# Performance work log

Hardware: AMD Instinct MI355X
Metric: run time of the kernel (lower is better)

Reference implementation:

```python
import jax, jax.numpy as jnp
import numpy as np
from jax import lax

CHUNK = 256  # points of the query set processed per step; intermediate is [B, CHUNK, M]


def _nn_min(x, y):
    """For each point in x [B,N,3], squared distance + index of nearest point in y [B,M,3].
    Chunked over N so the full [B,N,M] distance matrix is never materialized."""
    B, N, _ = x.shape
    y2 = jnp.sum(y * y, axis=-1)  # [B, M]
    K = N // CHUNK
    xr = jnp.swapaxes(x.reshape(B, K, CHUNK, 3), 0, 1)  # [K, B, CHUNK, 3]

    def chunk_fn(xc):  # xc: [B, CHUNK, 3]
        d = (jnp.sum(xc * xc, axis=-1)[..., None]
             - 2.0 * jnp.einsum('bcd,bmd->bcm', xc, y)
             + y2[:, None, :])  # [B, CHUNK, M]
        return jnp.min(d, axis=-1), jnp.argmin(d, axis=-1).astype(jnp.int32)

    dmin, idx = lax.map(chunk_fn, xr)  # [K, B, CHUNK]
    dmin = jnp.swapaxes(dmin, 0, 1).reshape(B, N)
    idx = jnp.swapaxes(idx, 0, 1).reshape(B, N)
    return dmin, idx


def setup_inputs() -> dict:
    key = jax.random.key(0)
    k1, k2 = jax.random.split(key)
    xyz1 = jax.random.normal(k1, (8, 16384, 3), dtype=jnp.float32)
    xyz2 = jax.random.normal(k2, (8, 16384, 3), dtype=jnp.float32)
    return {"xyz1": xyz1, "xyz2": xyz2}


def reference(xyz1, xyz2):
    dist1, idx1 = _nn_min(xyz1, xyz2)  # [B, N], [B, N]
    dist2, idx2 = _nn_min(xyz2, xyz1)  # [B, M], [B, M]
    return dist1, dist2, idx1, idx2
```

## Files before the change

### kernel.cpp

```cpp
#include <hip/hip_runtime.h>
#include <stdint.h>

#define BATCH 8
#define NPTS  16384
#define BN    (BATCH * NPTS)
#define NT    512
#define NTH   256
#define QPB   256
#define MARGIN 3.0e-3f

typedef float f32x16 __attribute__((ext_vector_type(16)));
typedef short s16x8  __attribute__((ext_vector_type(8)));

__device__ __forceinline__ uint16_t bfr(float x) {
    uint32_t u = __float_as_uint(x);
    return (uint16_t)((u + 0x7FFFu + ((u >> 16) & 1u)) >> 16);
}
__device__ __forceinline__ float bff(uint16_t s) {
    return __uint_as_float(((uint32_t)s) << 16);
}
__device__ __forceinline__ void split2(float v, uint16_t* a, uint16_t* b) {
    *a = bfr(v); *b = bfr(v - bff(*a));
}
__device__ __forceinline__ uint32_t pk2(uint16_t lo, uint16_t hi) {
    return (uint32_t)lo | ((uint32_t)hi << 16);
}
__device__ __forceinline__ uint32_t key32(float d) {
    uint32_t b = __float_as_uint(d);
    return (b & 0x80000000u) ? ~b : (b | 0x80000000u);
}
__device__ __forceinline__ float dec32(uint32_t k) {
    return __uint_as_float((k & 0x80000000u) ? (k ^ 0x80000000u) : ~k);
}

#define F16(M_) M_(0) M_(1) M_(2) M_(3) M_(4) M_(5) M_(6) M_(7) \
                M_(8) M_(9) M_(10) M_(11) M_(12) M_(13) M_(14) M_(15)

#define MIN3(a, b, c) fminf(fminf((a), (b)), (c))

__device__ __forceinline__ float fold16(const f32x16 a) {
    const float u0 = MIN3(a[0],  a[1],  a[2]);
    const float u1 = MIN3(a[3],  a[4],  a[5]);
    const float u2 = MIN3(a[6],  a[7],  a[8]);
    const float u3 = MIN3(a[9],  a[10], a[11]);
    const float u4 = MIN3(a[12], a[13], a[14]);
    const float v0 = MIN3(u0, u1, a[15]);
    const float v1 = MIN3(u2, u3, u4);
    return fminf(v0, v1);
}

__global__ __launch_bounds__(256) void enc_kernel(
    const float* __restrict__ Y, uint4* __restrict__ enc2,
    float4* __restrict__ y4)
{
#pragma clang fp contract(off)
    const int g = blockIdx.x * 256 + threadIdx.x;
    const int b = g >> 14, p = g & (NPTS - 1);
    const float y0 = Y[(size_t)g * 3 + 0];
    const float y1 = Y[(size_t)g * 3 + 1];
    const float y2 = Y[(size_t)g * 3 + 2];
    const float ys = (y0 * y0 + y1 * y1) + y2 * y2;
    uint16_t Ya, Yb; split2(ys, &Ya, &Yb);
    uint16_t H0, M0; split2(-2.0f * y0, &H0, &M0);
    uint16_t H1, M1; split2(-2.0f * y1, &H1, &M1);
    uint16_t H2, M2; split2(-2.0f * y2, &H2, &M2);
    const uint16_t ONE = 0x3F80;
    const int tile = p >> 5, col = p & 31;
    const size_t base = ((size_t)b * NT + tile) * 64;
    enc2[base + col]      = make_uint4(pk2(ONE, ONE), pk2(Ya, Yb), pk2(H0, M0), pk2(H0, M0));
    enc2[base + 32 + col] = make_uint4(pk2(H1, M1), pk2(H1, M1), pk2(H2, M2), pk2(H2, M2));
    y4[g] = make_float4(y0, y1, y2, ys);
}

#define MKQFR(dst, qq) { \
        const float* xp = Xp + (size_t)(qq) * 3; \
        const float x0 = xp[0], x1 = xp[1], x2 = xp[2]; \
        const float xs = (x0 * x0 + x1 * x1) + x2 * x2; \
        uint16_t Xa, Xb; split2(xs, &Xa, &Xb); \
        uint16_t h0, m0; split2(x0, &h0, &m0); \
        uint16_t h1, m1; split2(x1, &h1, &m1); \
        uint16_t h2, m2; split2(x2, &h2, &m2); \
        const uint16_t ONE = 0x3F80; \
        if (hi == 0) { \
            dst[0]=(short)Xa; dst[1]=(short)Xb; dst[2]=(short)ONE; dst[3]=(short)ONE; \
            dst[4]=(short)h0; dst[5]=(short)h0; dst[6]=(short)m0;  dst[7]=(short)m0; \
        } else { \
            dst[0]=(short)h1; dst[1]=(short)h1; dst[2]=(short)m1;  dst[3]=(short)m1; \
            dst[4]=(short)h2; dst[5]=(short)h2; dst[6]=(short)m2;  dst[7]=(short)m2; \
        } }

#define SWEEP_DECODE() \
    const int tid = threadIdx.x; \
    const int l   = tid & 63; \
    const int wv  = tid >> 6; \
    const int col = l & 31; \
    const int hi  = l >> 5; \
    const int batch = blockIdx.x & 7; \
    const int kh    = (blockIdx.x >> 3) & 1; \
    const int xblk  = blockIdx.x >> 4; \
    const int qbase = batch * NPTS + xblk * QPB + wv * 64; \
    const uint4* pb = enc2 + ((size_t)batch * NT + (size_t)kh * NTH) * 64;

__global__ __launch_bounds__(256, 4) void nn_sweep1(
    const float* __restrict__ Xp, const uint4* __restrict__ enc2,
    uint32_t* __restrict__ mkey)
{
#pragma clang fp contract(off)
    SWEEP_DECODE()

    const f32x16 zf = {0.f,0.f,0.f,0.f,0.f,0.f,0.f,0.f,
                       0.f,0.f,0.f,0.f,0.f,0.f,0.f,0.f};

    s16x8 qfr0, qfr1;
    MKQFR(qfr0, qbase + col)
    MKQFR(qfr1, qbase + 32 + col)

    float run0 = __builtin_inff(), run1 = __builtin_inff();

    uint4 n0 = pb[0 * 64 + l], n1 = pb[1 * 64 + l];
    uint4 n2 = pb[2 * 64 + l], n3 = pb[3 * 64 + l];
    for (int t = 0; t < NTH; t += 4) {
        const uint4 c0 = n0, c1 = n1, c2 = n2, c3 = n3;
        const uint4* nb = pb + (size_t)(t + 4) * 64;
        n0 = nb[0 * 64 + l]; n1 = nb[1 * 64 + l];
        n2 = nb[2 * 64 + l]; n3 = nb[3 * 64 + l];
#define S1T(cq) { \
        const s16x8 pA = __builtin_bit_cast(s16x8, cq); \
        const f32x16 a0 = __builtin_amdgcn_mfma_f32_32x32x16_bf16(pA, qfr0, zf, 0, 0, 0); \
        run0 = fminf(run0, fold16(a0)); \
        const f32x16 a1 = __builtin_amdgcn_mfma_f32_32x32x16_bf16(pA, qfr1, zf, 0, 0, 0); \
        run1 = fminf(run1, fold16(a1)); }
        S1T(c0) S1T(c1) S1T(c2) S1T(c3)
#undef S1T
    }
    run0 = fminf(run0, __shfl_xor(run0, 32, 64));
    run1 = fminf(run1, __shfl_xor(run1, 32, 64));
    if (hi == 0) {
        atomicMin(&mkey[qbase + col],      key32(run0));
        atomicMin(&mkey[qbase + 32 + col], key32(run1));
    }
}

__global__ __launch_bounds__(256, 4) void nn_sweep2(
    const float* __restrict__ Xp, const uint4* __restrict__ enc2,
    const float4* __restrict__ y4, const uint32_t* __restrict__ mkey,
    unsigned long long* __restrict__ gkeys)
{
#pragma clang fp contract(off)
    __shared__ unsigned long long keys[QPB];
    SWEEP_DECODE()

    const float4* Y4 = y4 + (size_t)batch * NPTS;

    keys[tid] = ~0ull;

    const f32x16 zf = {0.f,0.f,0.f,0.f,0.f,0.f,0.f,0.f,
                       0.f,0.f,0.f,0.f,0.f,0.f,0.f,0.f};

    int rowpack[4] = {0, 0, 0, 0};
    {
        s16x8 pa = {0,0,0,0,0,0,0,0}, pbq = {0,0,0,0,0,0,0,0};
        if (hi == 0) { pa[0] = (short)bfr((float)col); pbq[0] = (short)0x3F80; }
        const f32x16 rowp = __builtin_amdgcn_mfma_f32_32x32x16_bf16(pa, pbq, zf, 0, 0, 0);
#define PR(i) rowpack[(i) >> 2] |= ((int)rowp[i] & 0xFF) << (((i) & 3) * 8);
        F16(PR)
#undef PR
    }

    s16x8 qfr0, qfr1;
    float qa0, qa1, qa2, qas, qb0, qb1, qb2, qbs;
    {
        const float* xp = Xp + (size_t)(qbase + col) * 3;
        qa0 = xp[0]; qa1 = xp[1]; qa2 = xp[2];
        qas = (qa0 * qa0 + qa1 * qa1) + qa2 * qa2;
    }
    {
        const float* xp = Xp + (size_t)(qbase + 32 + col) * 3;
        qb0 = xp[0]; qb1 = xp[1]; qb2 = xp[2];
        qbs = (qb0 * qb0 + qb1 * qb1) + qb2 * qb2;
    }
    MKQFR(qfr0, qbase + col)
    MKQFR(qfr1, qbase + 32 + col)

    const float thr0 = dec32(mkey[qbase + col]) + MARGIN;
    const float thr1 = dec32(mkey[qbase + 32 + col]) + MARGIN;

    __syncthreads();

#define HITR(accv, jb, foff, thr, qx0, qx1, qx2, qxs, r) \
        if ((accv)[r] <= (thr)) { \
            const int jc = (jb) + ((rowpack[(r) >> 2] >> (((r) & 3) * 8)) & 0xFF); \
            const float4 yv = Y4[jc]; \
            const float dd = ((qxs) - 2.0f * (((qx0) * yv.x + (qx1) * yv.y) + (qx2) * yv.z)) + yv.w; \
            atomicMin(&keys[wv * 64 + (foff) + col], \
                      ((unsigned long long)key32(dd) << 32) | (uint32_t)jc); }
#define HIT(accv, jb, foff, thr, qx0, qx1, qx2, qxs) \
        if (fold16(accv) <= (thr)) { \
            HITR(accv, jb, foff, thr, qx0, qx1, qx2, qxs, 0) \
            HITR(accv, jb, foff, thr, qx0, qx1, qx2, qxs, 1) \
            HITR(accv, jb, foff, thr, qx0, qx1, qx2, qxs, 2) \
            HITR(accv, jb, foff, thr, qx0, qx1, qx2, qxs, 3) \
            HITR(accv, jb, foff, thr, qx0, qx1, qx2, qxs, 4) \
            HITR(accv, jb, foff, thr, qx0, qx1, qx2, qxs, 5) \
            HITR(accv, jb, foff, thr, qx0, qx1, qx2, qxs, 6) \
            HITR(accv, jb, foff, thr, qx0, qx1, qx2, qxs, 7) \
            HITR(accv, jb, foff, thr, qx0, qx1, qx2, qxs, 8) \
            HITR(accv, jb, foff, thr, qx0, qx1, qx2, qxs, 9) \
            HITR(accv, jb, foff, thr, qx0, qx1, qx2, qxs, 10) \
            HITR(accv, jb, foff, thr, qx0, qx1, qx2, qxs, 11) \
            HITR(accv, jb, foff, thr, qx0, qx1, qx2, qxs, 12) \
            HITR(accv, jb, foff, thr, qx0, qx1, qx2, qxs, 13) \
            HITR(accv, jb, foff, thr, qx0, qx1, qx2, qxs, 14) \
            HITR(accv, jb, foff, thr, qx0, qx1, qx2, qxs, 15) \
        }

    uint4 n0 = pb[0 * 64 + l], n1 = pb[1 * 64 + l];
    for (int t = 0; t < NTH; t += 2) {
        const uint4 c0 = n0, c1 = n1;
        const uint4* nb = pb + (size_t)(t + 2) * 64;
        n0 = nb[0 * 64 + l]; n1 = nb[1 * 64 + l];
#define S2T(cq, j) { \
        const s16x8 pA = __builtin_bit_cast(s16x8, cq); \
        const int jb = (kh * NTH + t + (j)) * 32; \
        const f32x16 a0 = __builtin_amdgcn_mfma_f32_32x32x16_bf16(pA, qfr0, zf, 0, 0, 0); \
        HIT(a0, jb, 0, thr0, qa0, qa1, qa2, qas) \
        const f32x16 a1 = __builtin_amdgcn_mfma_f32_32x32x16_bf16(pA, qfr1, zf, 0, 0, 0); \
        HIT(a1, jb, 32, thr1, qb0, qb1, qb2, qbs) }
        S2T(c0, 0) S2T(c1, 1)
#undef S2T
    }
#undef HIT
#undef HITR

    __syncthreads();
    {
        const unsigned long long m = keys[tid];
        atomicMin(&gkeys[(size_t)batch * NPTS + xblk * QPB + tid], m);
    }
}

__global__ __launch_bounds__(256) void writeout_k(
    const unsigned long long* __restrict__ gkeys, float* __restrict__ out, int dir)
{
    const size_t q = (size_t)blockIdx.x * 256 + threadIdx.x;
    const unsigned long long m = gkeys[q];
    out[(size_t)dir * BN + q]       = dec32((uint32_t)(m >> 32));
    out[(size_t)(2 + dir) * BN + q] = (float)(uint32_t)(m & 0xFFFFFFFFu);
}

extern "C" void kernel_launch(void* const* d_in, const int* in_sizes, int n_in,
                              void* d_out, int out_size, void* d_ws, size_t ws_size,
                              hipStream_t stream) {
    const float* xyz1 = (const float*)d_in[0];
    const float* xyz2 = (const float*)d_in[1];
    float* out = (float*)d_out;

    char* base = (char*)d_ws;
    uint4*    enc2 = (uint4*)base;
    float4*   y4   = (float4*)(base + (size_t)4 * 1024 * 1024);
    uint32_t* mkey = (uint32_t*)(base + (size_t)6 * 1024 * 1024);
    unsigned long long* gkeys =
        (unsigned long long*)(base + (size_t)6 * 1024 * 1024 + 512 * 1024);

    for (int dir = 0; dir < 2; ++dir) {
        const float* Xq = dir ? xyz2 : xyz1;
        const float* Yp = dir ? xyz1 : xyz2;

        hipMemsetAsync(mkey, 0xFF, (size_t)BN * 4, stream);
        hipMemsetAsync(gkeys, 0xFF, (size_t)BN * 8, stream);

        enc_kernel<<<BN / 256, 256, 0, stream>>>(Yp, enc2, y4);
        nn_sweep1<<<1024, 256, 0, stream>>>(Xq, enc2, mkey);
        nn_sweep2<<<1024, 256, 0, stream>>>(Xq, enc2, y4, mkey, gkeys);
        writeout_k<<<BN / 256, 256, 0, stream>>>(gkeys, out, dir);
    }
}
```

Baseline: 373.2 us.

## Merge both NN directions into single sweep launches and walk hit masks by ctz

Both query directions now run in one launch per stage. Each direction gets its own encoded buffers and key arrays, and the block index decodes dir, batch, half and block, which doubles the grid to 2048 blocks and cuts the number of launches and memsets. The second sweep also changes its hit check. It builds a 16-bit mask of candidate rows, then visits only the set bits with ctz, instead of a fold test followed by 16 unrolled branches. The aim is better GPU fill, less launch and tail overhead, and less divergent branching, at the cost of twice the workspace.

```diff
diff --git a/kernel.cpp b/kernel.cpp
--- a/kernel.cpp
+++ b/kernel.cpp
@@ -95,14 +95,18 @@
     const int wv  = tid >> 6; \
     const int col = l & 31; \
     const int hi  = l >> 5; \
-    const int batch = blockIdx.x & 7; \
-    const int kh    = (blockIdx.x >> 3) & 1; \
-    const int xblk  = blockIdx.x >> 4; \
-    const int qbase = batch * NPTS + xblk * QPB + wv * 64; \
-    const uint4* pb = enc2 + ((size_t)batch * NT + (size_t)kh * NTH) * 64;
+    int dir, batch, kh, xblk; \
+    { const int g = blockIdx.x; \
+      const int s = 2 * (g & 7) + ((g >> 3) & 1); \
+      dir = s >> 3; batch = s & 7; kh = (g >> 4) & 1; xblk = g >> 5; } \
+    const float* Xp = dir ? xyz2 : xyz1; \
+    const uint4* pb = (dir ? enc2B : enc2A) + \
+                      ((size_t)batch * NT + (size_t)kh * NTH) * 64; \
+    const int qbase = batch * NPTS + xblk * QPB + wv * 64;
 
 __global__ __launch_bounds__(256, 4) void nn_sweep1(
-    const float* __restrict__ Xp, const uint4* __restrict__ enc2,
+    const float* __restrict__ xyz1, const float* __restrict__ xyz2,
+    const uint4* __restrict__ enc2A, const uint4* __restrict__ enc2B,
     uint32_t* __restrict__ mkey)
 {
 #pragma clang fp contract(off)
@@ -136,33 +140,37 @@
     run0 = fminf(run0, __shfl_xor(run0, 32, 64));
     run1 = fminf(run1, __shfl_xor(run1, 32, 64));
     if (hi == 0) {
-        atomicMin(&mkey[qbase + col],      key32(run0));
-        atomicMin(&mkey[qbase + 32 + col], key32(run1));
+        uint32_t* mp = mkey + (size_t)dir * BN;
+        atomicMin(&mp[qbase + col],      key32(run0));
+        atomicMin(&mp[qbase + 32 + col], key32(run1));
     }
 }
 
 __global__ __launch_bounds__(256, 4) void nn_sweep2(
-    const float* __restrict__ Xp, const uint4* __restrict__ enc2,
-    const float4* __restrict__ y4, const uint32_t* __restrict__ mkey,
-    unsigned long long* __restrict__ gkeys)
+    const float* __restrict__ xyz1, const float* __restrict__ xyz2,
+    const uint4* __restrict__ enc2A, const uint4* __restrict__ enc2B,
+    const float4* __restrict__ y4A, const float4* __restrict__ y4B,
+    const uint32_t* __restrict__ mkey, unsigned long long* __restrict__ gkeys)
 {
 #pragma clang fp contract(off)
     __shared__ unsigned long long keys[QPB];
     SWEEP_DECODE()
 
-    const float4* Y4 = y4 + (size_t)batch * NPTS;
+    const float4* Y4 = (dir ? y4B : y4A) + (size_t)batch * NPTS;
 
     keys[tid] = ~0ull;
 
     const f32x16 zf = {0.f,0.f,0.f,0.f,0.f,0.f,0.f,0.f,
                        0.f,0.f,0.f,0.f,0.f,0.f,0.f,0.f};
 
-    int rowpack[4] = {0, 0, 0, 0};
+    uint64_t rplo = 0, rphi = 0;
     {
         s16x8 pa = {0,0,0,0,0,0,0,0}, pbq = {0,0,0,0,0,0,0,0};
         if (hi == 0) { pa[0] = (short)bfr((float)col); pbq[0] = (short)0x3F80; }
         const f32x16 rowp = __builtin_amdgcn_mfma_f32_32x32x16_bf16(pa, pbq, zf, 0, 0, 0);
-#define PR(i) rowpack[(i) >> 2] |= ((int)rowp[i] & 0xFF) << (((i) & 3) * 8);
+#define PR(i) { const uint64_t e_ = (uint64_t)((int)rowp[i] & 0xFF); \
+                if ((i) < 8) rplo |= e_ << ((i) * 8); \
+                else         rphi |= e_ << (((i) - 8) * 8); }
         F16(PR)
 #undef PR
     }
@@ -182,37 +190,27 @@
     MKQFR(qfr0, qbase + col)
     MKQFR(qfr1, qbase + 32 + col)
 
-    const float thr0 = dec32(mkey[qbase + col]) + MARGIN;
-    const float thr1 = dec32(mkey[qbase + 32 + col]) + MARGIN;
+    const uint32_t* mp = mkey + (size_t)dir * BN;
+    const float thr0 = dec32(mp[qbase + col]) + MARGIN;
+    const float thr1 = dec32(mp[qbase + 32 + col]) + MARGIN;
 
     __syncthreads();
 
-#define HITR(accv, jb, foff, thr, qx0, qx1, qx2, qxs, r) \
-        if ((accv)[r] <= (thr)) { \
-            const int jc = (jb) + ((rowpack[(r) >> 2] >> (((r) & 3) * 8)) & 0xFF); \
+#define WALK(accv, jb, foff, thr, qx0, qx1, qx2, qxs) { \
+        uint32_t msk = 0; \
+        _Pragma("unroll") \
+        for (int i_ = 0; i_ < 16; ++i_) \
+            msk |= ((accv)[i_] <= (thr)) ? (1u << i_) : 0u; \
+        while (msk) { \
+            const int r_ = __builtin_ctz(msk); \
+            msk &= msk - 1; \
+            const uint64_t rp_ = (r_ & 8) ? rphi : rplo; \
+            const int jc = (jb) + (int)((rp_ >> ((r_ & 7) * 8)) & 0xFF); \
             const float4 yv = Y4[jc]; \
             const float dd = ((qxs) - 2.0f * (((qx0) * yv.x + (qx1) * yv.y) + (qx2) * yv.z)) + yv.w; \
             atomicMin(&keys[wv * 64 + (foff) + col], \
-                      ((unsigned long long)key32(dd) << 32) | (uint32_t)jc); }
-#define HIT(accv, jb, foff, thr, qx0, qx1, qx2, qxs) \
-        if (fold16(accv) <= (thr)) { \
-            HITR(accv, jb, foff, thr, qx0, qx1, qx2, qxs, 0) \
-            HITR(accv, jb, foff, thr, qx0, qx1, qx2, qxs, 1) \
-            HITR(accv, jb, foff, thr, qx0, qx1, qx2, qxs, 2) \
-            HITR(accv, jb, foff, thr, qx0, qx1, qx2, qxs, 3) \
-            HITR(accv, jb, foff, thr, qx0, qx1, qx2, qxs, 4) \
-            HITR(accv, jb, foff, thr, qx0, qx1, qx2, qxs, 5) \
-            HITR(accv, jb, foff, thr, qx0, qx1, qx2, qxs, 6) \
-            HITR(accv, jb, foff, thr, qx0, qx1, qx2, qxs, 7) \
-            HITR(accv, jb, foff, thr, qx0, qx1, qx2, qxs, 8) \
-            HITR(accv, jb, foff, thr, qx0, qx1, qx2, qxs, 9) \
-            HITR(accv, jb, foff, thr, qx0, qx1, qx2, qxs, 10) \
-            HITR(accv, jb, foff, thr, qx0, qx1, qx2, qxs, 11) \
-            HITR(accv, jb, foff, thr, qx0, qx1, qx2, qxs, 12) \
-            HITR(accv, jb, foff, thr, qx0, qx1, qx2, qxs, 13) \
-            HITR(accv, jb, foff, thr, qx0, qx1, qx2, qxs, 14) \
-            HITR(accv, jb, foff, thr, qx0, qx1, qx2, qxs, 15) \
-        }
+                      ((unsigned long long)key32(dd) << 32) | (uint32_t)jc); \
+        } }
 
     uint4 n0 = pb[0 * 64 + l], n1 = pb[1 * 64 + l];
     for (int t = 0; t < NTH; t += 2) {
@@ -223,27 +221,28 @@
         const s16x8 pA = __builtin_bit_cast(s16x8, cq); \
         const int jb = (kh * NTH + t + (j)) * 32; \
         const f32x16 a0 = __builtin_amdgcn_mfma_f32_32x32x16_bf16(pA, qfr0, zf, 0, 0, 0); \
-        HIT(a0, jb, 0, thr0, qa0, qa1, qa2, qas) \
+        WALK(a0, jb, 0, thr0, qa0, qa1, qa2, qas) \
         const f32x16 a1 = __builtin_amdgcn_mfma_f32_32x32x16_bf16(pA, qfr1, zf, 0, 0, 0); \
-        HIT(a1, jb, 32, thr1, qb0, qb1, qb2, qbs) }
+        WALK(a1, jb, 32, thr1, qb0, qb1, qb2, qbs) }
         S2T(c0, 0) S2T(c1, 1)
 #undef S2T
     }
-#undef HIT
-#undef HITR
+#undef WALK
 
     __syncthreads();
     {
         const unsigned long long m = keys[tid];
-        atomicMin(&gkeys[(size_t)batch * NPTS + xblk * QPB + tid], m);
+        atomicMin(&gkeys[(size_t)dir * BN + batch * NPTS + xblk * QPB + tid], m);
     }
 }
 
 __global__ __launch_bounds__(256) void writeout_k(
-    const unsigned long long* __restrict__ gkeys, float* __restrict__ out, int dir)
-{
-    const size_t q = (size_t)blockIdx.x * 256 + threadIdx.x;
-    const unsigned long long m = gkeys[q];
+    const unsigned long long* __restrict__ gkeys, float* __restrict__ out)
+{
+    const size_t i = (size_t)blockIdx.x * 256 + threadIdx.x;
+    const unsigned long long m = gkeys[i];
+    const int dir = (int)(i / BN);
+    const size_t q = i - (size_t)dir * BN;
     out[(size_t)dir * BN + q]       = dec32((uint32_t)(m >> 32));
     out[(size_t)(2 + dir) * BN + q] = (float)(uint32_t)(m & 0xFFFFFFFFu);
 }
@@ -256,22 +255,20 @@
     float* out = (float*)d_out;
 
     char* base = (char*)d_ws;
-    uint4*    enc2 = (uint4*)base;
-    float4*   y4   = (float4*)(base + (size_t)4 * 1024 * 1024);
-    uint32_t* mkey = (uint32_t*)(base + (size_t)6 * 1024 * 1024);
+    uint4*    enc2A = (uint4*)base;
+    uint4*    enc2B = (uint4*)(base + (size_t)4 * 1024 * 1024);
+    float4*   y4A   = (float4*)(base + (size_t)8 * 1024 * 1024);
+    float4*   y4B   = (float4*)(base + (size_t)10 * 1024 * 1024);
+    uint32_t* mkey  = (uint32_t*)(base + (size_t)12 * 1024 * 1024);
     unsigned long long* gkeys =
-        (unsigned long long*)(base + (size_t)6 * 1024 * 1024 + 512 * 1024);
-
-    for (int dir = 0; dir < 2; ++dir) {
-        const float* Xq = dir ? xyz2 : xyz1;
-        const float* Yp = dir ? xyz1 : xyz2;
-
-        hipMemsetAsync(mkey, 0xFF, (size_t)BN * 4, stream);
-        hipMemsetAsync(gkeys, 0xFF, (size_t)BN * 8, stream);
-
-        enc_kernel<<<BN / 256, 256, 0, stream>>>(Yp, enc2, y4);
-        nn_sweep1<<<1024, 256, 0, stream>>>(Xq, enc2, mkey);
-        nn_sweep2<<<1024, 256, 0, stream>>>(Xq, enc2, y4, mkey, gkeys);
-        writeout_k<<<BN / 256, 256, 0, stream>>>(gkeys, out, dir);
-    }
-}
+        (unsigned long long*)(base + (size_t)13 * 1024 * 1024);
+
+    enc_kernel<<<BN / 256, 256, 0, stream>>>(xyz2, enc2A, y4A);
+    enc_kernel<<<BN / 256, 256, 0, stream>>>(xyz1, enc2B, y4B);
+    hipMemsetAsync(mkey, 0xFF, (size_t)3 * 1024 * 1024, stream);
+
+    nn_sweep1<<<2048, 256, 0, stream>>>(xyz1, xyz2, enc2A, enc2B, mkey);
+    nn_sweep2<<<2048, 256, 0, stream>>>(xyz1, xyz2, enc2A, enc2B,
+                                        y4A, y4B, mkey, gkeys);
+    writeout_k<<<(2 * BN) / 256, 256, 0, stream>>>(gkeys, out);
+}
```

Result: slower. 487.7 us (+30.7%).
